# Kernel optimization log

Hardware: AMD Instinct MI355X
Metric: run time of the kernel (lower is better)

Reference implementation:

```python
import jax, jax.numpy as jnp
import numpy as np

B, T, L = 16384, 128, 9  # batch, padded seq len, num tags


def setup_inputs() -> dict:
    key = jax.random.key(0)
    k1, k2, k3, k4 = jax.random.split(key, 4)
    logits = jax.random.normal(k1, (B, T, L), dtype=jnp.float32)
    labels = jax.random.randint(k2, (B, T), 0, L, dtype=jnp.int32)
    seq_lens = jax.random.randint(k3, (B,), 1, T + 1, dtype=jnp.int32)
    trans = jax.random.uniform(k4, (L, L), dtype=jnp.float32)
    return {"logits": logits, "labels": labels, "seq_lens": seq_lens, "trans": trans}


def _crf_neg_log_likelihood_sum(logits, labels, seq_lens, trans):
    # Faithful port of tfa.text.crf_log_likelihood; loss = sum(-log_likelihood).
    Bn, Tn, Ln = logits.shape
    mask = (jnp.arange(Tn)[None, :] < seq_lens[:, None]).astype(logits.dtype)  # [B,T]

    # --- sequence score: unary + binary (transition) terms ---
    unary = jnp.take_along_axis(logits, labels[..., None].astype(jnp.int32), axis=-1)[..., 0]  # [B,T]
    unary = jnp.sum(unary * mask, axis=1)  # [B]
    btrans = trans[labels[:, :-1], labels[:, 1:]]  # [B,T-1]
    binary = jnp.sum(btrans * mask[:, 1:], axis=1)  # [B]
    seq_score = unary + binary

    # --- log partition via forward algorithm (scan over time) ---
    logits_t = jnp.swapaxes(logits, 0, 1)  # [T,B,L]
    mask_t = jnp.swapaxes(mask, 0, 1) > 0  # [T,B] bool

    def step(alphas, xs):
        lt, mt = xs  # lt: [B,L] emissions at t, mt: [B] valid mask
        # alphas[b,i] + trans[i,j] -> logsumexp over i, plus emission j
        new = jax.nn.logsumexp(alphas[:, :, None] + trans[None, :, :], axis=1) + lt
        return jnp.where(mt[:, None], new, alphas), None

    alphas0 = logits_t[0]  # [B,L]
    alphas, _ = jax.lax.scan(step, alphas0, (logits_t[1:], mask_t[1:]))
    log_norm = jax.nn.logsumexp(alphas, axis=-1)  # [B]

    log_likelihood = seq_score - log_norm
    return -jnp.sum(log_likelihood)


def reference(logits, labels, seq_lens, trans):
    return _crf_neg_log_likelihood_sum(logits, labels, seq_lens, trans)
```

## Files before the change

kernel.cpp:

```cpp
#include <hip/hip_runtime.h>

constexpr int T = 128;
constexpr int L = 9;
constexpr float LOG2E = 1.4426950408889634f;
constexpr float LN2   = 0.6931471805599453f;

__device__ __forceinline__ float fexp2(float x){float r;asm("v_exp_f32 %0, %1":"=v"(r):"v"(x));return r;}
__device__ __forceinline__ float flog2(float x){float r;asm("v_log_f32 %0, %1":"=v"(r):"v"(x));return r;}

#define DO_ROW(M,i) M(i,0) M(i,1) M(i,2) M(i,3) M(i,4) M(i,5) M(i,6) M(i,7) M(i,8)
#define DO_ALL(M) DO_ROW(M,0) DO_ROW(M,1) DO_ROW(M,2) DO_ROW(M,3) DO_ROW(M,4) DO_ROW(M,5) DO_ROW(M,6) DO_ROW(M,7) DO_ROW(M,8)
#define REP9(M) M(0) M(1) M(2) M(3) M(4) M(5) M(6) M(7) M(8)

#define DECL_ET(i,j) float et_##i##_##j;
#define INIT_ET(i,j) et_##i##_##j = __int_as_float(__builtin_amdgcn_readfirstlane(__float_as_int(fexp2(trans[(i)*9+(j)] * LOG2E))));

#define DECLQ(B,i0,i1,i2,i3) float B##_##i0, B##_##i1, B##_##i2, B##_##i3;
#define DECL_BUF(B) DECLQ(B,0,1,2,3) DECLQ(B,4,5,6,7) DECLQ(B,8,9,10,11) \
  DECLQ(B,12,13,14,15) DECLQ(B,16,17,18,19) DECLQ(B,20,21,22,23) \
  DECLQ(B,24,25,26,27) DECLQ(B,28,29,30,31) DECLQ(B,32,33,34,35)

#define LOADQ(B,q,i0,i1,i2,i3) { const float4 t_ = p_[q]; B##_##i0=t_.x; B##_##i1=t_.y; B##_##i2=t_.z; B##_##i3=t_.w; }
#define LOAD_BLK(B,bk,LABV) { const float4* p_ = reinterpret_cast<const float4*>(gRow + (bk)*36); \
  LOADQ(B,0,0,1,2,3) LOADQ(B,1,4,5,6,7) LOADQ(B,2,8,9,10,11) \
  LOADQ(B,3,12,13,14,15) LOADQ(B,4,16,17,18,19) LOADQ(B,5,20,21,22,23) \
  LOADQ(B,6,24,25,26,27) LOADQ(B,7,28,29,30,31) LOADQ(B,8,32,33,34,35) \
  LABV = *reinterpret_cast<const int4*>(gLab + (bk)*4); }

#define LGS(B,O0,O1,O2,O3,O4,O5,O6,O7,O8) \
  const float lg_0=B##_##O0, lg_1=B##_##O1, lg_2=B##_##O2, lg_3=B##_##O3, lg_4=B##_##O4, \
              lg_5=B##_##O5, lg_6=B##_##O6, lg_7=B##_##O7, lg_8=B##_##O8;

#define USEL const float x0_=(lab_&1)?lg_1:lg_0, x1_=(lab_&1)?lg_3:lg_2, x2_=(lab_&1)?lg_5:lg_4, x3_=(lab_&1)?lg_7:lg_6; \
  const float y0_=(lab_&2)?x1_:x0_, y1_=(lab_&2)?x3_:x2_; \
  const float z0_=(lab_&4)?y1_:y0_; \
  const float usel_=(lab_&8)?lg_8:z0_;

#define EXPJ(j) const float el_##j = fexp2(lg_##j * LOG2E);
#define MACC(j) float s_##j = a_0*et_0_##j; \
  s_##j=fmaf(a_1,et_1_##j,s_##j); s_##j=fmaf(a_2,et_2_##j,s_##j); s_##j=fmaf(a_3,et_3_##j,s_##j); \
  s_##j=fmaf(a_4,et_4_##j,s_##j); s_##j=fmaf(a_5,et_5_##j,s_##j); s_##j=fmaf(a_6,et_6_##j,s_##j); \
  s_##j=fmaf(a_7,et_7_##j,s_##j); s_##j=fmaf(a_8,et_8_##j,s_##j);
#define AUPD(j) a_##j = upd_ ? s_##j*el_##j : a_##j;

#define STEP_T(B,O0,O1,O2,O3,O4,O5,O6,O7,O8,LAB,BSEL,UPDEXPR) { \
  const int lab_ = (LAB); const bool upd_ = (UPDEXPR); \
  LGS(B,O0,O1,O2,O3,O4,O5,O6,O7,O8) \
  USEL \
  REP9(EXPJ) \
  REP9(MACC) \
  REP9(AUPD) \
  unary  += upd_ ? usel_ : 0.0f; \
  binary += upd_ ? (BSEL) : 0.0f; }

#define STEP_FIRST(B,LAB) { \
  const int lab_ = (LAB); \
  LGS(B,0,1,2,3,4,5,6,7,8) \
  USEL \
  a_0=fexp2(lg_0*LOG2E); a_1=fexp2(lg_1*LOG2E); a_2=fexp2(lg_2*LOG2E); \
  a_3=fexp2(lg_3*LOG2E); a_4=fexp2(lg_4*LOG2E); a_5=fexp2(lg_5*LOG2E); \
  a_6=fexp2(lg_6*LOG2E); a_7=fexp2(lg_7*LOG2E); a_8=fexp2(lg_8*LOG2E); \
  unary += usel_; }

#define RESCALE { const unsigned ua_=__float_as_uint(a_0); const int k_=(int)(ua_>>23)-127; \
  const float sc_=__uint_as_float((254u-(ua_>>23))<<23); \
  a_0*=sc_; a_1*=sc_; a_2*=sc_; a_3*=sc_; a_4*=sc_; a_5*=sc_; a_6*=sc_; a_7*=sc_; a_8*=sc_; E+=k_; }

#define COMPUTE4(B,LABV,T0) { \
  const int l0_=(LABV).x, l1_=(LABV).y, l2_=(LABV).z, l3_=(LABV).w; \
  const float bs0_=sTrans[plab*9+l0_], bs1_=sTrans[l0_*9+l1_], bs2_=sTrans[l1_*9+l2_], bs3_=sTrans[l2_*9+l3_]; \
  STEP_T(B,0,1,2,3,4,5,6,7,8,l0_,bs0_,(((T0)+0)<len)) \
  STEP_T(B,9,10,11,12,13,14,15,16,17,l1_,bs1_,(((T0)+1)<len)) \
  STEP_T(B,18,19,20,21,22,23,24,25,26,l2_,bs2_,(((T0)+2)<len)) \
  STEP_T(B,27,28,29,30,31,32,33,34,35,l3_,bs3_,(((T0)+3)<len)) \
  plab = l3_; \
  RESCALE }

#define COMPUTE4_FIRST(B,LABV) { \
  const int l0_=(LABV).x, l1_=(LABV).y, l2_=(LABV).z, l3_=(LABV).w; \
  const float bs1_=sTrans[l0_*9+l1_], bs2_=sTrans[l1_*9+l2_], bs3_=sTrans[l2_*9+l3_]; \
  STEP_FIRST(B,l0_) \
  STEP_T(B,9,10,11,12,13,14,15,16,17,l1_,bs1_,(1<len)) \
  STEP_T(B,18,19,20,21,22,23,24,25,26,l2_,bs2_,(2<len)) \
  STEP_T(B,27,28,29,30,31,32,33,34,35,l3_,bs3_,(3<len)) \
  plab = l3_; \
  RESCALE }

__global__ void __launch_bounds__(64, 1)
crf_kernel(const float* __restrict__ logits,
           const int* __restrict__ labels,
           const int* __restrict__ seq_lens,
           const float* __restrict__ trans,
           float* __restrict__ out)
{
    __shared__ float sTrans[81];
    const int lane = threadIdx.x;
    const int b = blockIdx.x * 64 + lane;

    for (int i = lane; i < 81; i += 64) sTrans[i] = trans[i];
    __syncthreads();

    DO_ALL(DECL_ET)
    DO_ALL(INIT_ET)

    const int len = seq_lens[b];
    const float* gRow = logits + (long)b * (T * L);
    const int*   gLab = labels + (long)b * T;

    int maxlen = len;
#pragma unroll
    for (int off = 32; off > 0; off >>= 1)
        maxlen = max(maxlen, __shfl_xor(maxlen, off, 64));

    float a_0=0.f,a_1=0.f,a_2=0.f,a_3=0.f,a_4=0.f,a_5=0.f,a_6=0.f,a_7=0.f,a_8=0.f;
    float unary = 0.f, binary = 0.f;
    int E = 0, plab = 0;

    DECL_BUF(bufA)
    DECL_BUF(bufB)
    int4 labA, labB;

    LOAD_BLK(bufA,0,labA);
    LOAD_BLK(bufB,1,labB);
    COMPUTE4_FIRST(bufA,labA);

#pragma unroll 1
    for (int i = 1; i < 31; i += 2) {
        if (i * 4 >= maxlen) break;
        LOAD_BLK(bufA,i+1,labA);
        COMPUTE4(bufB,labB,i*4);
        LOAD_BLK(bufB,i+2,labB);
        COMPUTE4(bufA,labA,(i+1)*4);
    }
    if (124 < maxlen)
        COMPUTE4(bufB,labB,124);

    const float ssum = a_0+a_1+a_2+a_3+a_4+a_5+a_6+a_7+a_8;
    float nll = LN2 * (flog2(ssum) + (float)E) - unary - binary;

#pragma unroll
    for (int off = 32; off > 0; off >>= 1) nll += __shfl_down(nll, off, 64);
    if (lane == 0) atomicAdd(out, nll);
}

extern "C" void kernel_launch(void* const* d_in, const int* in_sizes, int n_in,
                              void* d_out, int out_size, void* d_ws, size_t ws_size,
                              hipStream_t stream)
{
    const float* logits   = (const float*)d_in[0];
    const int*   labels   = (const int*)d_in[1];
    const int*   seq_lens = (const int*)d_in[2];
    const float* trans    = (const float*)d_in[3];
    float* out = (float*)d_out;

    const int B = in_sizes[2];
    hipMemsetAsync(d_out, 0, sizeof(float), stream);
    crf_kernel<<<dim3(B / 64), dim3(64), 0, stream>>>(logits, labels, seq_lens, trans, out);
}
```

Baseline: 151.8 us.

## Stage logits and labels through LDS via async global_load_lds double buffering

Replaces the register double buffer of per-block logits and label loads with direct global-to-LDS async loads (global_load_lds, 16 bytes) into a two-slot shared staging buffer. Explicit vmcnt waits keep one block's loads in flight while the other is consumed. The goal is to free VGPRs and overlap memory latency with the recurrence. The cost is extra LDS reads each step and reliance on hand-placed waitcnt. The per-block copy from LDS to each lane reads with the lane index, so the layout has to match what global_load_lds writes per lane, and that mapping is subtle.

Measured after the change: 156.7 us. +3.2%, slower.

```diff
diff --git a/kernel.cpp b/kernel.cpp
--- a/kernel.cpp
+++ b/kernel.cpp
@@ -8,24 +8,17 @@
 __device__ __forceinline__ float fexp2(float x){float r;asm("v_exp_f32 %0, %1":"=v"(r):"v"(x));return r;}
 __device__ __forceinline__ float flog2(float x){float r;asm("v_log_f32 %0, %1":"=v"(r):"v"(x));return r;}
 
+__device__ __forceinline__ void gl_lds16(const void* g, void* l) {
+    __builtin_amdgcn_global_load_lds((const __attribute__((address_space(1))) unsigned*)g,
+                                     (__attribute__((address_space(3))) unsigned*)l, 16, 0, 0);
+}
+
 #define DO_ROW(M,i) M(i,0) M(i,1) M(i,2) M(i,3) M(i,4) M(i,5) M(i,6) M(i,7) M(i,8)
 #define DO_ALL(M) DO_ROW(M,0) DO_ROW(M,1) DO_ROW(M,2) DO_ROW(M,3) DO_ROW(M,4) DO_ROW(M,5) DO_ROW(M,6) DO_ROW(M,7) DO_ROW(M,8)
 #define REP9(M) M(0) M(1) M(2) M(3) M(4) M(5) M(6) M(7) M(8)
 
 #define DECL_ET(i,j) float et_##i##_##j;
 #define INIT_ET(i,j) et_##i##_##j = __int_as_float(__builtin_amdgcn_readfirstlane(__float_as_int(fexp2(trans[(i)*9+(j)] * LOG2E))));
-
-#define DECLQ(B,i0,i1,i2,i3) float B##_##i0, B##_##i1, B##_##i2, B##_##i3;
-#define DECL_BUF(B) DECLQ(B,0,1,2,3) DECLQ(B,4,5,6,7) DECLQ(B,8,9,10,11) \
-  DECLQ(B,12,13,14,15) DECLQ(B,16,17,18,19) DECLQ(B,20,21,22,23) \
-  DECLQ(B,24,25,26,27) DECLQ(B,28,29,30,31) DECLQ(B,32,33,34,35)
-
-#define LOADQ(B,q,i0,i1,i2,i3) { const float4 t_ = p_[q]; B##_##i0=t_.x; B##_##i1=t_.y; B##_##i2=t_.z; B##_##i3=t_.w; }
-#define LOAD_BLK(B,bk,LABV) { const float4* p_ = reinterpret_cast<const float4*>(gRow + (bk)*36); \
-  LOADQ(B,0,0,1,2,3) LOADQ(B,1,4,5,6,7) LOADQ(B,2,8,9,10,11) \
-  LOADQ(B,3,12,13,14,15) LOADQ(B,4,16,17,18,19) LOADQ(B,5,20,21,22,23) \
-  LOADQ(B,6,24,25,26,27) LOADQ(B,7,28,29,30,31) LOADQ(B,8,32,33,34,35) \
-  LABV = *reinterpret_cast<const int4*>(gLab + (bk)*4); }
 
 #define LGS(B,O0,O1,O2,O3,O4,O5,O6,O7,O8) \
   const float lg_0=B##_##O0, lg_1=B##_##O1, lg_2=B##_##O2, lg_3=B##_##O3, lg_4=B##_##O4, \
@@ -86,6 +79,37 @@
   plab = l3_; \
   RESCALE }
 
+#define PREFETCH(bk,bufsel) { \
+  const float* gsrc_ = gRow + (bk)*36; \
+  gl_lds16(gsrc_+ 0, &stage[bufsel][0][0]); \
+  gl_lds16(gsrc_+ 4, &stage[bufsel][1][0]); \
+  gl_lds16(gsrc_+ 8, &stage[bufsel][2][0]); \
+  gl_lds16(gsrc_+12, &stage[bufsel][3][0]); \
+  gl_lds16(gsrc_+16, &stage[bufsel][4][0]); \
+  gl_lds16(gsrc_+20, &stage[bufsel][5][0]); \
+  gl_lds16(gsrc_+24, &stage[bufsel][6][0]); \
+  gl_lds16(gsrc_+28, &stage[bufsel][7][0]); \
+  gl_lds16(gsrc_+32, &stage[bufsel][8][0]); \
+  gl_lds16(gLab + (bk)*4, &labStage[bufsel][0]); }
+
+#define WAIT_KEEP10 { asm volatile("s_waitcnt vmcnt(10)" ::: "memory"); __builtin_amdgcn_sched_barrier(0); }
+#define WAIT_ALL    { asm volatile("s_waitcnt vmcnt(0)"  ::: "memory"); __builtin_amdgcn_sched_barrier(0); }
+
+#define LDS_BLK(B,bufsel,LABV) \
+  const float4 B##c0_=stage[bufsel][0][lane], B##c1_=stage[bufsel][1][lane], B##c2_=stage[bufsel][2][lane], \
+               B##c3_=stage[bufsel][3][lane], B##c4_=stage[bufsel][4][lane], B##c5_=stage[bufsel][5][lane], \
+               B##c6_=stage[bufsel][6][lane], B##c7_=stage[bufsel][7][lane], B##c8_=stage[bufsel][8][lane]; \
+  const float B##_0 =B##c0_.x, B##_1 =B##c0_.y, B##_2 =B##c0_.z, B##_3 =B##c0_.w, \
+              B##_4 =B##c1_.x, B##_5 =B##c1_.y, B##_6 =B##c1_.z, B##_7 =B##c1_.w, \
+              B##_8 =B##c2_.x, B##_9 =B##c2_.y, B##_10=B##c2_.z, B##_11=B##c2_.w, \
+              B##_12=B##c3_.x, B##_13=B##c3_.y, B##_14=B##c3_.z, B##_15=B##c3_.w, \
+              B##_16=B##c4_.x, B##_17=B##c4_.y, B##_18=B##c4_.z, B##_19=B##c4_.w, \
+              B##_20=B##c5_.x, B##_21=B##c5_.y, B##_22=B##c5_.z, B##_23=B##c5_.w, \
+              B##_24=B##c6_.x, B##_25=B##c6_.y, B##_26=B##c6_.z, B##_27=B##c6_.w, \
+              B##_28=B##c7_.x, B##_29=B##c7_.y, B##_30=B##c7_.z, B##_31=B##c7_.w, \
+              B##_32=B##c8_.x, B##_33=B##c8_.y, B##_34=B##c8_.z, B##_35=B##c8_.w; \
+  const int4 LABV = labStage[bufsel][lane];
+
 __global__ void __launch_bounds__(64, 1)
 crf_kernel(const float* __restrict__ logits,
            const int* __restrict__ labels,
@@ -93,7 +117,9 @@
            const float* __restrict__ trans,
            float* __restrict__ out)
 {
-    __shared__ float sTrans[81];
+    __shared__ float4 stage[2][9][64];
+    __shared__ int4   labStage[2][64];
+    __shared__ float  sTrans[81];
     const int lane = threadIdx.x;
     const int b = blockIdx.x * 64 + lane;
 
@@ -111,29 +137,29 @@
 #pragma unroll
     for (int off = 32; off > 0; off >>= 1)
         maxlen = max(maxlen, __shfl_xor(maxlen, off, 64));
+    const int nblk = (maxlen + 3) >> 2;
 
     float a_0=0.f,a_1=0.f,a_2=0.f,a_3=0.f,a_4=0.f,a_5=0.f,a_6=0.f,a_7=0.f,a_8=0.f;
     float unary = 0.f, binary = 0.f;
     int E = 0, plab = 0;
 
-    DECL_BUF(bufA)
-    DECL_BUF(bufB)
-    int4 labA, labB;
+    PREFETCH(0, 0);
+    if (nblk > 1) { PREFETCH(1, 1); WAIT_KEEP10 }
+    else          { WAIT_ALL }
+    {
+        LDS_BLK(b0, 0, lab0)
+        COMPUTE4_FIRST(b0, lab0)
+    }
 
-    LOAD_BLK(bufA,0,labA);
-    LOAD_BLK(bufB,1,labB);
-    COMPUTE4_FIRST(bufA,labA);
-
+    int buf = 1;
 #pragma unroll 1
-    for (int i = 1; i < 31; i += 2) {
-        if (i * 4 >= maxlen) break;
-        LOAD_BLK(bufA,i+1,labA);
-        COMPUTE4(bufB,labB,i*4);
-        LOAD_BLK(bufB,i+2,labB);
-        COMPUTE4(bufA,labA,(i+1)*4);
+    for (int bk = 1; bk < nblk; ++bk) {
+        if (bk + 1 < nblk) { PREFETCH(bk + 1, buf ^ 1); WAIT_KEEP10 }
+        else               { WAIT_ALL }
+        LDS_BLK(cb, buf, clab)
+        COMPUTE4(cb, clab, bk * 4)
+        buf ^= 1;
     }
-    if (124 < maxlen)
-        COMPUTE4(bufB,labB,124);
 
     const float ssum = a_0+a_1+a_2+a_3+a_4+a_5+a_6+a_7+a_8;
     float nll = LN2 * (flog2(ssum) + (float)E) - unary - binary;
```
